# Kernel optimization log

Measured on AMD Instinct MI355X. Metric: run time of the kernel, lower is better.

Reference implementation:

```python
import jax, jax.numpy as jnp
import numpy as np

N, E, F_IN, ED, H, C, G, ACT = 50000, 800000, 32, 5, 2, 32, 128, 8
HC = H * C


def _glorot(key, shape):
    fan_in, fan_out = shape[0], shape[-1]
    lim = (6.0 / (fan_in + fan_out)) ** 0.5
    return jax.random.uniform(key, shape, jnp.float32, -lim, lim)


def setup_inputs() -> dict:
    key = jax.random.key(0)
    ks = jax.random.split(key, 32)
    inp = {
        "x": jax.random.normal(ks[0], (N, F_IN), jnp.float32),
        "edge_index": jax.random.randint(ks[1], (2, E), 0, N, jnp.int64),
        "edge_attr": jax.random.normal(ks[2], (E, ED), jnp.float32),
        "batch": jnp.sort(jax.random.randint(ks[3], (N,), 0, G, jnp.int64)),
    }
    ki = 4
    for l, din in zip((1, 2, 3), (F_IN, HC, HC)):
        inp[f"W{l}"] = _glorot(ks[ki], (din, HC)); ki += 1
        inp[f"We{l}"] = _glorot(ks[ki], (ED, HC)); ki += 1
        inp[f"as{l}"] = _glorot(ks[ki], (H, C)); ki += 1
        inp[f"ad{l}"] = _glorot(ks[ki], (H, C)); ki += 1
        inp[f"ae{l}"] = _glorot(ks[ki], (H, C)); ki += 1
        inp[f"b{l}"] = jnp.zeros((HC,), jnp.float32)
    inp["Wl"] = _glorot(ks[ki], (HC, ACT)); ki += 1
    inp["bl"] = jnp.zeros((ACT,), jnp.float32)
    return inp


def _add_self_loops(edge_index, edge_attr):
    # PyG add_self_loops with fill_value='mean': self-loop edge_attr at node i
    # is the mean of edge_attr of edges whose dst is i (0 if none).
    dst = edge_index[1]
    deg = jax.ops.segment_sum(jnp.ones((E,), jnp.float32), dst, num_segments=N)
    loop_attr = jax.ops.segment_sum(edge_attr, dst, num_segments=N) / jnp.clip(deg, 1.0)[:, None]
    loops = jnp.arange(N, dtype=edge_index.dtype)
    ei = jnp.concatenate([edge_index, jnp.stack([loops, loops])], axis=1)
    ea = jnp.concatenate([edge_attr, loop_attr], axis=0)
    return ei, ea


def _gat_layer(x, src, dst, ea, W, We, a_s, a_d, a_e, b):
    xs = (x @ W).reshape(N, H, C)                      # node features per head
    e = (ea @ We).reshape(-1, H, C)                    # edge features per head
    a_src = jnp.einsum('nhc,hc->nh', xs, a_s)
    a_dst = jnp.einsum('nhc,hc->nh', xs, a_d)
    a_edge = jnp.einsum('ehc,hc->eh', e, a_e)
    logits = jax.nn.leaky_relu(a_src[src] + a_dst[dst] + a_edge, 0.2)  # [E',H]
    m = jax.ops.segment_max(logits, dst, num_segments=N)
    m = jnp.where(jnp.isfinite(m), m, 0.0)
    ex = jnp.exp(logits - m[dst])
    den = jax.ops.segment_sum(ex, dst, num_segments=N)
    alpha = ex / (den[dst] + 1e-16)
    msg = xs[src] * alpha[..., None]                   # [E',H,C]
    out = jax.ops.segment_sum(msg, dst, num_segments=N).reshape(N, HC)
    return out + b


def reference(x, edge_index, edge_attr, batch,
              W1, We1, as1, ad1, ae1, b1,
              W2, We2, as2, ad2, ae2, b2,
              W3, We3, as3, ad3, ae3, b3,
              Wl, bl):
    ei, ea = _add_self_loops(edge_index, edge_attr)
    src, dst = ei[0], ei[1]
    h = jax.nn.relu(_gat_layer(x, src, dst, ea, W1, We1, as1, ad1, ae1, b1))
    h = jax.nn.relu(_gat_layer(h, src, dst, ea, W2, We2, as2, ad2, ae2, b2))
    h = _gat_layer(h, src, dst, ea, W3, We3, as3, ad3, ae3, b3)
    # global mean pool over graphs
    cnt = jax.ops.segment_sum(jnp.ones((N,), jnp.float32), batch, num_segments=G)
    pooled = jax.ops.segment_sum(h, batch, num_segments=G) / jnp.clip(cnt, 1.0)[:, None]
    return jnp.tanh(pooled @ Wl + bl)
```

## Files before the change

kernel.cpp:

```cpp
#include <hip/hip_runtime.h>
#include <math.h>

#define N_NODES 50000
#define N_EDGES 800000
#define E_DIM   5
#define N_G     128
#define N_ACT   8
#define SBLK    512
#define SNB     ((N_NODES + SBLK - 1) / SBLK)


__global__ __launch_bounds__(256) void setup_kernel(
    const int* __restrict__ ei, const int* __restrict__ batch,
    const float* __restrict__ We1, const float* __restrict__ ae1,
    const float* __restrict__ We2, const float* __restrict__ ae2,
    const float* __restrict__ We3, const float* __restrict__ ae3,
    float* __restrict__ weff, int* __restrict__ gstart, int* __restrict__ hist) {
    int bid = blockIdx.x, tid = threadIdx.x;
    if (bid == 0) {
        if (tid <= N_G) {
            int g = tid, lo = 0, hi = N_NODES;
            while (lo < hi) { int mid = (lo + hi) >> 1; if (batch[mid] < g) lo = mid + 1; else hi = mid; }
            gstart[g] = lo;
        }
        int t = tid - 160;
        if (t >= 0 && t < 30) {
            int l = t / 10, r = t % 10, d = r >> 1, h = r & 1;
            const float* We = (l == 0) ? We1 : (l == 1) ? We2 : We3;
            const float* ae = (l == 0) ? ae1 : (l == 1) ? ae2 : ae3;
            float s = 0.f;
            for (int c = 0; c < 32; ++c) s += We[d * 64 + h * 32 + c] * ae[h * 32 + c];
            weff[l * 10 + d * 2 + h] = s;
        }
        return;
    }
    int k = (bid - 1) * 256 + tid;
    if (k < N_EDGES) atomicAdd(&hist[ei[N_EDGES + k]], 1);
}

__device__ __forceinline__ int wave_incl_scan(int v, int lane) {
    #pragma unroll
    for (int off = 1; off < 64; off <<= 1) {
        int n = __shfl_up(v, off);
        if (lane >= off) v += n;
    }
    return v;
}

__global__ __launch_bounds__(SBLK) void scan_bsum_kernel(const int* __restrict__ hist,
                                                         int* __restrict__ bsum) {
    int i = blockIdx.x * SBLK + threadIdx.x;
    int v = (i < N_NODES) ? hist[i] : 0;
    __shared__ int sm[SBLK / 64];
    int lane = threadIdx.x & 63, w = threadIdx.x >> 6;
    #pragma unroll
    for (int o = 32; o; o >>= 1) v += __shfl_xor(v, o);
    if (lane == 0) sm[w] = v;
    __syncthreads();
    if (threadIdx.x == 0) {
        int s = 0;
        #pragma unroll
        for (int k = 0; k < SBLK / 64; ++k) s += sm[k];
        bsum[blockIdx.x] = s;
    }
}

__global__ __launch_bounds__(SBLK) void scan_rowptr_kernel(const int* __restrict__ hist,
                                                           const int* __restrict__ bsum,
                                                           int* __restrict__ rowptr) {
    __shared__ int s_boffs;
    __shared__ int wtot[SBLK / 64];
    int bid = blockIdx.x;
    if (threadIdx.x < 64) {
        int v = 0;
        for (int i = threadIdx.x; i < bid; i += 64) v += bsum[i];
        #pragma unroll
        for (int o = 32; o; o >>= 1) v += __shfl_xor(v, o);
        if (threadIdx.x == 0) s_boffs = v;
    }
    int i = bid * SBLK + threadIdx.x;
    int v = (i < N_NODES) ? hist[i] : 0;
    int lane = threadIdx.x & 63, w = threadIdx.x >> 6;
    int inc = wave_incl_scan(v, lane);
    if (lane == 63) wtot[w] = inc;
    __syncthreads();
    int woff = 0;
    for (int k = 0; k < w; ++k) woff += wtot[k];
    int excl = s_boffs + woff + inc - v;
    if (i < N_NODES) rowptr[i] = excl;
    if (i == N_NODES - 1) rowptr[N_NODES] = excl + v;
}

__global__ void scatterA_kernel(const int* __restrict__ ei, const float* __restrict__ ea,
                                const float* __restrict__ weff,
                                const int* __restrict__ rowptr, int* __restrict__ cur,
                                float* __restrict__ recE, int* __restrict__ iperm) {
    int k = blockIdx.x * blockDim.x + threadIdx.x;
    if (k >= N_EDGES) return;
    int s = ei[k], d = ei[N_EDGES + k];
    const float* ep = ea + (size_t)k * E_DIM;
    float e[5];
    #pragma unroll
    for (int j = 0; j < 5; ++j) e[j] = ep[j];
    float r[6] = {0.f, 0.f, 0.f, 0.f, 0.f, 0.f};
    #pragma unroll
    for (int j = 0; j < 5; ++j) {
        r[0] += e[j] * weff[j * 2];      r[1] += e[j] * weff[j * 2 + 1];
        r[2] += e[j] * weff[10 + j * 2]; r[3] += e[j] * weff[10 + j * 2 + 1];
        r[4] += e[j] * weff[20 + j * 2]; r[5] += e[j] * weff[20 + j * 2 + 1];
    }
    float4* rp = (float4*)(recE + (size_t)k * 8);
    rp[0] = make_float4(r[0], r[1], r[2], r[3]);
    rp[1] = make_float4(r[4], r[5], __int_as_float(s), 0.f);
    int pos = rowptr[d] + atomicAdd(&cur[d], 1);
    iperm[pos] = k;
}

__global__ void gatherB_kernel(const int* __restrict__ iperm, const float* __restrict__ recE,
                               float* __restrict__ rec) {
    int pos = blockIdx.x * blockDim.x + threadIdx.x;
    if (pos >= N_EDGES) return;
    int k = iperm[pos];
    const float4* sp = (const float4*)(recE + (size_t)k * 8);
    float4 r0 = sp[0];
    float4 r1 = sp[1];
    float4* dp = (float4*)(rec + (size_t)pos * 8);
    dp[0] = r0;
    dp[1] = r1;
}


template <int DIN>
__global__ __launch_bounds__(256) void feat_kernel(
    const float* __restrict__ in, const float* __restrict__ W,
    const float* __restrict__ a_s, const float* __restrict__ a_d,
    float* __restrict__ xs, float* __restrict__ a_srcv, float* __restrict__ a_dstv) {
    __shared__ float Wl[DIN * 64];
    __shared__ float asl[64], adl[64];
    int tid = threadIdx.x;
    {
        const float4* Wg = (const float4*)W;
        float4* Wl4 = (float4*)Wl;
        #pragma unroll
        for (int i = tid; i < DIN * 16; i += 256) Wl4[i] = Wg[i];
        if (tid < 64) { asl[tid] = a_s[tid]; adl[tid] = a_d[tid]; }
    }
    __syncthreads();
    int n = blockIdx.x * 64 + (tid >> 2);
    int strip = tid & 3;
    if (n >= N_NODES) return;
    float4 xr[DIN / 4];
    const float4* row4 = (const float4*)(in + (size_t)n * DIN);
    #pragma unroll
    for (int k4 = 0; k4 < DIN / 4; ++k4) xr[k4] = row4[k4];
    float4 acc[4];
    #pragma unroll
    for (int j = 0; j < 4; ++j) acc[j] = make_float4(0.f, 0.f, 0.f, 0.f);
    const float4* W4 = (const float4*)Wl;
    #pragma unroll
    for (int k4 = 0; k4 < DIN / 4; ++k4) {
        float xk[4] = {xr[k4].x, xr[k4].y, xr[k4].z, xr[k4].w};
        #pragma unroll
        for (int kk = 0; kk < 4; ++kk) {
            int k = k4 * 4 + kk;
            #pragma unroll
            for (int j = 0; j < 4; ++j) {
                float4 w = W4[k * 16 + strip * 4 + j];
                acc[j].x += xk[kk] * w.x; acc[j].y += xk[kk] * w.y;
                acc[j].z += xk[kk] * w.z; acc[j].w += xk[kk] * w.w;
            }
        }
    }
    float ps = 0.f, pd = 0.f;
    #pragma unroll
    for (int j = 0; j < 4; ++j) {
        int c = strip * 16 + j * 4;
        ps += acc[j].x * asl[c] + acc[j].y * asl[c + 1] + acc[j].z * asl[c + 2] + acc[j].w * asl[c + 3];
        pd += acc[j].x * adl[c] + acc[j].y * adl[c + 1] + acc[j].z * adl[c + 2] + acc[j].w * adl[c + 3];
    }
    ps += __shfl_xor(ps, 1);
    pd += __shfl_xor(pd, 1);
    if ((strip & 1) == 0) {
        int h = strip >> 1;
        a_srcv[n * 2 + h] = ps;
        a_dstv[n * 2 + h] = pd;
    }
    float4* o = (float4*)(xs + (size_t)n * 64 + strip * 16);
    #pragma unroll
    for (int j = 0; j < 4; ++j) o[j] = acc[j];
}

template <int L>
__global__ __launch_bounds__(256) void node_agg_kernel(
    const int* __restrict__ rowptr, const float* __restrict__ rec,
    const float* __restrict__ a_srcv, const float* __restrict__ a_dstv,
    const float* __restrict__ xs, const float* __restrict__ b,
    float* __restrict__ out, int relu) {
    int nid = (blockIdx.x * 256 + threadIdx.x) >> 4;
    if (nid >= N_NODES) return;
    int lane = threadIdx.x & 63;
    int fl = lane & 15, h = fl >> 3;
    int gbase = lane & 48;
    int beg = rowptr[nid], end = rowptr[nid + 1];
    float2 ad2 = ((const float2*)a_dstv)[nid];
    float m0 = -INFINITY, m1 = -INFINITY;
    float4 acc = make_float4(0.f, 0.f, 0.f, 0.f);
    float den0 = 0.f, den1 = 0.f;
    float aes0 = 0.f, aes1 = 0.f;
    for (int cb = beg; cb < end; cb += 16) {
        int j = cb + fl;
        float l0 = -INFINITY, l1 = -INFINITY;
        int s = 0;
        if (j < end) {
            const float4* rp = (const float4*)(rec + (size_t)j * 8);
            float4 r0 = rp[0];
            float4 r1 = rp[1];
            s = __float_as_int(r1.z);
            float aex = (L == 0) ? r0.x : (L == 1) ? r0.z : r1.x;
            float aey = (L == 0) ? r0.y : (L == 1) ? r0.w : r1.y;
            aes0 += aex; aes1 += aey;
            float2 as2 = ((const float2*)a_srcv)[s];
            l0 = as2.x + ad2.x + aex;
            l1 = as2.y + ad2.y + aey;
            l0 = (l0 > 0.f) ? l0 : 0.2f * l0;
            l1 = (l1 > 0.f) ? l1 : 0.2f * l1;
        }
        float c0 = l0, c1 = l1;
        #pragma unroll
        for (int o = 8; o; o >>= 1) {
            c0 = fmaxf(c0, __shfl_xor(c0, o));
            c1 = fmaxf(c1, __shfl_xor(c1, o));
        }
        float n0 = fmaxf(m0, c0), n1 = fmaxf(m1, c1);
        float sc0 = expf(m0 - n0), sc1 = expf(m1 - n1);
        den0 *= sc0; den1 *= sc1;
        float sa = h ? sc1 : sc0;
        acc.x *= sa; acc.y *= sa; acc.z *= sa; acc.w *= sa;
        m0 = n0; m1 = n1;
        float ex0 = expf(l0 - m0);
        float ex1 = expf(l1 - m1);
        den0 += ex0; den1 += ex1;
        int cnt = min(end - cb, 16);
        for (int t4 = 0; t4 < cnt; t4 += 4) {
            int tA = gbase + t4;
            float eA0 = __shfl(ex0, tA),     eA1 = __shfl(ex1, tA);     int sA = __shfl(s, tA);
            float eB0 = __shfl(ex0, tA + 1), eB1 = __shfl(ex1, tA + 1); int sB = __shfl(s, tA + 1);
            float eC0 = __shfl(ex0, tA + 2), eC1 = __shfl(ex1, tA + 2); int sC = __shfl(s, tA + 2);
            float eD0 = __shfl(ex0, tA + 3), eD1 = __shfl(ex1, tA + 3); int sD = __shfl(s, tA + 3);
            float eA = h ? eA1 : eA0, eB = h ? eB1 : eB0;
            float eC = h ? eC1 : eC0, eD = h ? eD1 : eD0;
            float4 xa = *(const float4*)(xs + (size_t)sA * 64 + fl * 4);
            float4 xb = *(const float4*)(xs + (size_t)sB * 64 + fl * 4);
            float4 xc = *(const float4*)(xs + (size_t)sC * 64 + fl * 4);
            float4 xd = *(const float4*)(xs + (size_t)sD * 64 + fl * 4);
            acc.x += eA * xa.x + eB * xb.x + eC * xc.x + eD * xd.x;
            acc.y += eA * xa.y + eB * xb.y + eC * xc.y + eD * xd.y;
            acc.z += eA * xa.z + eB * xb.z + eC * xc.z + eD * xd.z;
            acc.w += eA * xa.w + eB * xb.w + eC * xc.w + eD * xd.w;
        }
    }
    #pragma unroll
    for (int o = 8; o; o >>= 1) {
        den0 += __shfl_xor(den0, o); den1 += __shfl_xor(den1, o);
        aes0 += __shfl_xor(aes0, o); aes1 += __shfl_xor(aes1, o);
    }
    int ne = end - beg;
    float aeS = (h ? aes1 : aes0) / fmaxf((float)ne, 1.f);
    float2 as2 = ((const float2*)a_srcv)[nid];
    float ls = (h ? as2.y + ad2.y : as2.x + ad2.x) + aeS;
    ls = (ls > 0.f) ? ls : 0.2f * ls;
    float mh = h ? m1 : m0;
    float nm = fmaxf(mh, ls);
    float sc = expf(mh - nm);
    float exS = expf(ls - nm);
    float den = (h ? den1 : den0) * sc + exS;
    float4 xv = *(const float4*)(xs + (size_t)nid * 64 + fl * 4);
    float inv = 1.f / (den + 1e-16f);
    float4 b4 = ((const float4*)b)[fl];
    float4 v;
    v.x = (acc.x * sc + exS * xv.x) * inv + b4.x;
    v.y = (acc.y * sc + exS * xv.y) * inv + b4.y;
    v.z = (acc.z * sc + exS * xv.z) * inv + b4.z;
    v.w = (acc.w * sc + exS * xv.w) * inv + b4.w;
    if (relu) {
        v.x = fmaxf(v.x, 0.f); v.y = fmaxf(v.y, 0.f);
        v.z = fmaxf(v.z, 0.f); v.w = fmaxf(v.w, 0.f);
    }
    ((float4*)(out + (size_t)nid * 64))[fl] = v;
}


__global__ __launch_bounds__(256) void pool_head_kernel(
    const float* __restrict__ hfeat, const int* __restrict__ gstart,
    const float* __restrict__ Wl, const float* __restrict__ bl,
    float* __restrict__ out) {
    __shared__ float sm[4][64];
    __shared__ float pooledL[64];
    int g = blockIdx.x;
    int w = threadIdx.x >> 6, lane = threadIdx.x & 63;
    int beg = gstart[g], end = gstart[g + 1];
    float acc = 0.f;
    for (int n = beg + w; n < end; n += 4)
        acc += hfeat[(size_t)n * 64 + lane];
    sm[w][lane] = acc;
    __syncthreads();
    if (w == 0) {
        float v = sm[0][lane] + sm[1][lane] + sm[2][lane] + sm[3][lane];
        pooledL[lane] = v / fmaxf((float)(end - beg), 1.f);
    }
    __syncthreads();
    if (threadIdx.x < N_ACT) {
        int a = threadIdx.x;
        float s = bl[a];
        #pragma unroll
        for (int j = 0; j < 64; ++j) s += pooledL[j] * Wl[j * 8 + a];
        out[g * N_ACT + a] = tanhf(s);
    }
}

extern "C" void kernel_launch(void* const* d_in, const int* in_sizes, int n_in,
                              void* d_out, int out_size, void* d_ws, size_t ws_size,
                              hipStream_t stream) {
    const float* x    = (const float*)d_in[0];
    const int*   ei   = (const int*)d_in[1];
    const float* ea   = (const float*)d_in[2];
    const int*   batch= (const int*)d_in[3];
    const float* W[3]   = {(const float*)d_in[4],  (const float*)d_in[10], (const float*)d_in[16]};
    const float* We[3]  = {(const float*)d_in[5],  (const float*)d_in[11], (const float*)d_in[17]};
    const float* as_[3] = {(const float*)d_in[6],  (const float*)d_in[12], (const float*)d_in[18]};
    const float* ad_[3] = {(const float*)d_in[7],  (const float*)d_in[13], (const float*)d_in[19]};
    const float* ae_[3] = {(const float*)d_in[8],  (const float*)d_in[14], (const float*)d_in[20]};
    const float* b_[3]  = {(const float*)d_in[9],  (const float*)d_in[15], (const float*)d_in[21]};
    const float* Wlin = (const float*)d_in[22];
    const float* bl   = (const float*)d_in[23];
    float* out = (float*)d_out;

    float* ws = (float*)d_ws;
    size_t off = 0;
    float* A      = ws + off; off += (size_t)N_NODES * 64;
    float* B      = ws + off; off += (size_t)N_NODES * 64;
    float* recE   = A;
    float* rec    = ws + off; off += (size_t)N_EDGES * 8;
    float* a_srcv = ws + off; off += N_NODES * 2;
    float* a_dstv = ws + off; off += N_NODES * 2;
    float* weff   = ws + off; off += 32;
    int* rowptr = (int*)(ws + off); off += N_NODES + 1;
    int* hist   = (int*)(ws + off); off += N_NODES;
    int* cur    = (int*)(ws + off); off += N_NODES;
    int* gstart = (int*)(ws + off); off += N_G + 1;
    int* bsum   = (int*)(ws + off); off += SNB;
    int* iperm  = (int*)(ws + off); off += N_EDGES;

    hipMemsetAsync(hist, 0, 2 * N_NODES * sizeof(int), stream);
    setup_kernel<<<1 + (N_EDGES + 255) / 256, 256, 0, stream>>>(
        ei, batch, We[0], ae_[0], We[1], ae_[1], We[2], ae_[2], weff, gstart, hist);
    scan_bsum_kernel<<<SNB, SBLK, 0, stream>>>(hist, bsum);
    scan_rowptr_kernel<<<SNB, SBLK, 0, stream>>>(hist, bsum, rowptr);
    scatterA_kernel<<<(N_EDGES + 255) / 256, 256, 0, stream>>>(ei, ea, weff, rowptr, cur,
                                                               recE, iperm);
    gatherB_kernel<<<(N_EDGES + 255) / 256, 256, 0, stream>>>(iperm, recE, rec);

    const int NB = (N_NODES * 16 + 255) / 256;
    const int FB = (N_NODES + 63) / 64;
    for (int l = 0; l < 3; ++l) {
        if (l == 0)
            feat_kernel<32><<<FB, 256, 0, stream>>>(x, W[0], as_[0], ad_[0], B, a_srcv, a_dstv);
        else
            feat_kernel<64><<<FB, 256, 0, stream>>>(A, W[l], as_[l], ad_[l], B, a_srcv, a_dstv);
        if (l == 0)
            node_agg_kernel<0><<<NB, 256, 0, stream>>>(rowptr, rec, a_srcv, a_dstv, B, b_[0], A, 1);
        else if (l == 1)
            node_agg_kernel<1><<<NB, 256, 0, stream>>>(rowptr, rec, a_srcv, a_dstv, B, b_[1], A, 1);
        else
            node_agg_kernel<2><<<NB, 256, 0, stream>>>(rowptr, rec, a_srcv, a_dstv, B, b_[2], A, 0);
    }
    pool_head_kernel<<<N_G, 256, 0, stream>>>(A, gstart, Wlin, bl, out);
}
```

Measured before the change: 405.3 us.

## Scatter edge records directly and use two-pass softmax in node aggregation

The CSR build now writes each edge's 32-byte record straight to its sorted slot, which removes the iperm array and the separate gather kernel along with its extra read and write of the edge records. The node aggregation kernel changes from a single-pass online softmax to two passes. The first pass computes per-lane running max and denominator, merges them across lanes with shuffles, and folds in the self-loop term. The second pass then accumulates messages with the final max, so the per-chunk shuffle reductions and accumulator rescaling are gone, and expf is replaced by __expf. In exchange the edge records and a_src are read twice per layer, and the scattered 32-byte writes are less coalesced.

```diff
diff --git a/kernel.cpp b/kernel.cpp
--- a/kernel.cpp
+++ b/kernel.cpp
@@ -91,10 +91,10 @@
     if (i == N_NODES - 1) rowptr[N_NODES] = excl + v;
 }
 
-__global__ void scatterA_kernel(const int* __restrict__ ei, const float* __restrict__ ea,
-                                const float* __restrict__ weff,
-                                const int* __restrict__ rowptr, int* __restrict__ cur,
-                                float* __restrict__ recE, int* __restrict__ iperm) {
+__global__ void scatter_kernel(const int* __restrict__ ei, const float* __restrict__ ea,
+                               const float* __restrict__ weff,
+                               const int* __restrict__ rowptr, int* __restrict__ cur,
+                               float* __restrict__ rec) {
     int k = blockIdx.x * blockDim.x + threadIdx.x;
     if (k >= N_EDGES) return;
     int s = ei[k], d = ei[N_EDGES + k];
@@ -109,24 +109,10 @@
         r[2] += e[j] * weff[10 + j * 2]; r[3] += e[j] * weff[10 + j * 2 + 1];
         r[4] += e[j] * weff[20 + j * 2]; r[5] += e[j] * weff[20 + j * 2 + 1];
     }
-    float4* rp = (float4*)(recE + (size_t)k * 8);
+    int pos = rowptr[d] + atomicAdd(&cur[d], 1);
+    float4* rp = (float4*)(rec + (size_t)pos * 8);
     rp[0] = make_float4(r[0], r[1], r[2], r[3]);
     rp[1] = make_float4(r[4], r[5], __int_as_float(s), 0.f);
-    int pos = rowptr[d] + atomicAdd(&cur[d], 1);
-    iperm[pos] = k;
-}
-
-__global__ void gatherB_kernel(const int* __restrict__ iperm, const float* __restrict__ recE,
-                               float* __restrict__ rec) {
-    int pos = blockIdx.x * blockDim.x + threadIdx.x;
-    if (pos >= N_EDGES) return;
-    int k = iperm[pos];
-    const float4* sp = (const float4*)(recE + (size_t)k * 8);
-    float4 r0 = sp[0];
-    float4 r1 = sp[1];
-    float4* dp = (float4*)(rec + (size_t)pos * 8);
-    dp[0] = r0;
-    dp[1] = r1;
 }
 
 
@@ -203,13 +189,60 @@
     int gbase = lane & 48;
     int beg = rowptr[nid], end = rowptr[nid + 1];
     float2 ad2 = ((const float2*)a_dstv)[nid];
-    float m0 = -INFINITY, m1 = -INFINITY;
+
+    float m0 = -INFINITY, m1 = -INFINITY, d0 = 0.f, d1 = 0.f;
+    float aes0 = 0.f, aes1 = 0.f;
+    for (int j = beg + fl; j < end; j += 16) {
+        const float4* rp = (const float4*)(rec + (size_t)j * 8);
+        float4 r0 = rp[0];
+        float4 r1 = rp[1];
+        int s = __float_as_int(r1.z);
+        float aex = (L == 0) ? r0.x : (L == 1) ? r0.z : r1.x;
+        float aey = (L == 0) ? r0.y : (L == 1) ? r0.w : r1.y;
+        aes0 += aex; aes1 += aey;
+        float2 as2 = ((const float2*)a_srcv)[s];
+        float l0 = as2.x + ad2.x + aex;
+        float l1 = as2.y + ad2.y + aey;
+        l0 = (l0 > 0.f) ? l0 : 0.2f * l0;
+        l1 = (l1 > 0.f) ? l1 : 0.2f * l1;
+        float n0 = fmaxf(m0, l0);
+        d0 = d0 * __expf(m0 - n0) + __expf(l0 - n0); m0 = n0;
+        float n1 = fmaxf(m1, l1);
+        d1 = d1 * __expf(m1 - n1) + __expf(l1 - n1); m1 = n1;
+    }
+    #pragma unroll
+    for (int o = 8; o; o >>= 1) {
+        float mo0 = __shfl_xor(m0, o), do0 = __shfl_xor(d0, o);
+        float mo1 = __shfl_xor(m1, o), do1 = __shfl_xor(d1, o);
+        float n0 = fmaxf(m0, mo0);
+        float ea0 = (m0 == n0) ? 1.f : __expf(m0 - n0);
+        float eb0 = (mo0 == n0) ? 1.f : __expf(mo0 - n0);
+        d0 = d0 * ea0 + do0 * eb0; m0 = n0;
+        float n1 = fmaxf(m1, mo1);
+        float ea1 = (m1 == n1) ? 1.f : __expf(m1 - n1);
+        float eb1 = (mo1 == n1) ? 1.f : __expf(mo1 - n1);
+        d1 = d1 * ea1 + do1 * eb1; m1 = n1;
+        aes0 += __shfl_xor(aes0, o);
+        aes1 += __shfl_xor(aes1, o);
+    }
+    int ne = end - beg;
+    float invne = 1.f / fmaxf((float)ne, 1.f);
+    float2 as2n = ((const float2*)a_srcv)[nid];
+    float ls0 = as2n.x + ad2.x + aes0 * invne;
+    float ls1 = as2n.y + ad2.y + aes1 * invne;
+    ls0 = (ls0 > 0.f) ? ls0 : 0.2f * ls0;
+    ls1 = (ls1 > 0.f) ? ls1 : 0.2f * ls1;
+    float M0 = fmaxf(m0, ls0), M1 = fmaxf(m1, ls1);
+    float sc0 = (m0 == M0) ? 1.f : __expf(m0 - M0);
+    float sc1 = (m1 == M1) ? 1.f : __expf(m1 - M1);
+    float exS0 = __expf(ls0 - M0), exS1 = __expf(ls1 - M1);
+    float den0 = d0 * sc0 + exS0;
+    float den1 = d1 * sc1 + exS1;
+
     float4 acc = make_float4(0.f, 0.f, 0.f, 0.f);
-    float den0 = 0.f, den1 = 0.f;
-    float aes0 = 0.f, aes1 = 0.f;
     for (int cb = beg; cb < end; cb += 16) {
         int j = cb + fl;
-        float l0 = -INFINITY, l1 = -INFINITY;
+        float ex0 = 0.f, ex1 = 0.f;
         int s = 0;
         if (j < end) {
             const float4* rp = (const float4*)(rec + (size_t)j * 8);
@@ -218,28 +251,14 @@
             s = __float_as_int(r1.z);
             float aex = (L == 0) ? r0.x : (L == 1) ? r0.z : r1.x;
             float aey = (L == 0) ? r0.y : (L == 1) ? r0.w : r1.y;
-            aes0 += aex; aes1 += aey;
             float2 as2 = ((const float2*)a_srcv)[s];
-            l0 = as2.x + ad2.x + aex;
-            l1 = as2.y + ad2.y + aey;
+            float l0 = as2.x + ad2.x + aex;
+            float l1 = as2.y + ad2.y + aey;
             l0 = (l0 > 0.f) ? l0 : 0.2f * l0;
             l1 = (l1 > 0.f) ? l1 : 0.2f * l1;
-        }
-        float c0 = l0, c1 = l1;
-        #pragma unroll
-        for (int o = 8; o; o >>= 1) {
-            c0 = fmaxf(c0, __shfl_xor(c0, o));
-            c1 = fmaxf(c1, __shfl_xor(c1, o));
-        }
-        float n0 = fmaxf(m0, c0), n1 = fmaxf(m1, c1);
-        float sc0 = expf(m0 - n0), sc1 = expf(m1 - n1);
-        den0 *= sc0; den1 *= sc1;
-        float sa = h ? sc1 : sc0;
-        acc.x *= sa; acc.y *= sa; acc.z *= sa; acc.w *= sa;
-        m0 = n0; m1 = n1;
-        float ex0 = expf(l0 - m0);
-        float ex1 = expf(l1 - m1);
-        den0 += ex0; den1 += ex1;
+            ex0 = __expf(l0 - M0);
+            ex1 = __expf(l1 - M1);
+        }
         int cnt = min(end - cb, 16);
         for (int t4 = 0; t4 < cnt; t4 += 4) {
             int tA = gbase + t4;
@@ -259,29 +278,16 @@
             acc.w += eA * xa.w + eB * xb.w + eC * xc.w + eD * xd.w;
         }
     }
-    #pragma unroll
-    for (int o = 8; o; o >>= 1) {
-        den0 += __shfl_xor(den0, o); den1 += __shfl_xor(den1, o);
-        aes0 += __shfl_xor(aes0, o); aes1 += __shfl_xor(aes1, o);
-    }
-    int ne = end - beg;
-    float aeS = (h ? aes1 : aes0) / fmaxf((float)ne, 1.f);
-    float2 as2 = ((const float2*)a_srcv)[nid];
-    float ls = (h ? as2.y + ad2.y : as2.x + ad2.x) + aeS;
-    ls = (ls > 0.f) ? ls : 0.2f * ls;
-    float mh = h ? m1 : m0;
-    float nm = fmaxf(mh, ls);
-    float sc = expf(mh - nm);
-    float exS = expf(ls - nm);
-    float den = (h ? den1 : den0) * sc + exS;
+    float exSh = h ? exS1 : exS0;
+    float den  = (h ? den1 : den0) + 1e-16f;
     float4 xv = *(const float4*)(xs + (size_t)nid * 64 + fl * 4);
-    float inv = 1.f / (den + 1e-16f);
+    float inv = 1.f / den;
     float4 b4 = ((const float4*)b)[fl];
     float4 v;
-    v.x = (acc.x * sc + exS * xv.x) * inv + b4.x;
-    v.y = (acc.y * sc + exS * xv.y) * inv + b4.y;
-    v.z = (acc.z * sc + exS * xv.z) * inv + b4.z;
-    v.w = (acc.w * sc + exS * xv.w) * inv + b4.w;
+    v.x = (acc.x + exSh * xv.x) * inv + b4.x;
+    v.y = (acc.y + exSh * xv.y) * inv + b4.y;
+    v.z = (acc.z + exSh * xv.z) * inv + b4.z;
+    v.w = (acc.w + exSh * xv.w) * inv + b4.w;
     if (relu) {
         v.x = fmaxf(v.x, 0.f); v.y = fmaxf(v.y, 0.f);
         v.z = fmaxf(v.z, 0.f); v.w = fmaxf(v.w, 0.f);
@@ -339,7 +345,6 @@
     size_t off = 0;
     float* A      = ws + off; off += (size_t)N_NODES * 64;
     float* B      = ws + off; off += (size_t)N_NODES * 64;
-    float* recE   = A;
     float* rec    = ws + off; off += (size_t)N_EDGES * 8;
     float* a_srcv = ws + off; off += N_NODES * 2;
     float* a_dstv = ws + off; off += N_NODES * 2;
@@ -349,16 +354,13 @@
     int* cur    = (int*)(ws + off); off += N_NODES;
     int* gstart = (int*)(ws + off); off += N_G + 1;
     int* bsum   = (int*)(ws + off); off += SNB;
-    int* iperm  = (int*)(ws + off); off += N_EDGES;
 
     hipMemsetAsync(hist, 0, 2 * N_NODES * sizeof(int), stream);
     setup_kernel<<<1 + (N_EDGES + 255) / 256, 256, 0, stream>>>(
         ei, batch, We[0], ae_[0], We[1], ae_[1], We[2], ae_[2], weff, gstart, hist);
     scan_bsum_kernel<<<SNB, SBLK, 0, stream>>>(hist, bsum);
     scan_rowptr_kernel<<<SNB, SBLK, 0, stream>>>(hist, bsum, rowptr);
-    scatterA_kernel<<<(N_EDGES + 255) / 256, 256, 0, stream>>>(ei, ea, weff, rowptr, cur,
-                                                               recE, iperm);
-    gatherB_kernel<<<(N_EDGES + 255) / 256, 256, 0, stream>>>(iperm, recE, rec);
+    scatter_kernel<<<(N_EDGES + 255) / 256, 256, 0, stream>>>(ei, ea, weff, rowptr, cur, rec);
 
     const int NB = (N_NODES * 16 + 255) / 256;
     const int FB = (N_NODES + 63) / 64;
```

Result: faster. 391.5 us (-3.4%).
